# Kernel tuning notes

Hardware: AMD Instinct MI355X
Metric: run time of the kernel (lower is better)

## Reference

```python
import jax, jax.numpy as jnp
import numpy as np

H = 60.0  # self.h
C = jnp.array([10665991.0, 27000000.0, 7953253.0], dtype=jnp.float32)  # self.c (9e6*3 = 27e6)


def setup_inputs() -> dict:
    key = jax.random.key(0)
    k1, k2, k3 = jax.random.split(key, 3)
    B, T = 8192, 1024
    # room temperatures in Kelvin, strictly positive (model uses 1/x)
    x0 = 280.0 + 20.0 * jax.random.uniform(k1, (B, 3), dtype=jnp.float32)
    u = jax.random.uniform(k2, (B, T, 8), dtype=jnp.float32)
    # col 0: external temperature ~[250,300] K; cols 1..7: positive power/irradiation
    u = u.at[:, :, 0].set(250.0 + 50.0 * u[:, :, 0])
    u = u.at[:, :, 1:].multiply(1000.0)
    # 14 scalar log-conductance params: [l12, l23, le1..3, ls1..3, lh1..3, lc1..3]
    lam = 0.1 * jax.random.normal(k3, (14,), dtype=jnp.float32)
    return {"x0": x0, "u": u, "lam": lam}


def _forward(x0, u, lam):
    e = jnp.exp(lam)
    e12, e23 = e[0], e[1]
    ee, es, eh, ec = e[2:5], e[5:8], e[8:11], e[11:14]  # each [3]

    def step(x, ut):  # x: [B,3], ut: [B,8]
        inv = 1.0 / x
        d12 = inv[:, 0] - inv[:, 1]
        d23 = inv[:, 1] - inv[:, 2]
        # A @ x^T, with A's only nonzeros at (0,1),(1,0),(1,2),(2,1)
        Ax = jnp.stack([
            e12 * d12 * x[:, 1],
            -e12 * d12 * x[:, 0] + e23 * d23 * x[:, 2],
            -e23 * d23 * x[:, 1],
        ], axis=-1)  # [B,3]
        u0 = ut[:, 0:1]  # external temperature
        # B @ u_t: external exchange + solar + per-room heating (u2..4) + cooling (u5..7)
        Bu = (ee * (inv - 1.0 / u0) * u0
              + es * ut[:, 1:2]
              + eh * ut[:, 2:5]
              + ec * ut[:, 5:8])  # [B,3]
        x_new = x * jnp.exp(H * (Ax + Bu) / C)
        return x_new, x_new

    # loop runs for T-1 steps using u[:, t] for t = 0..T-2
    u_seq = jnp.swapaxes(u[:, :-1, :], 0, 1)  # [T-1, B, 8]
    _, xs = jax.lax.scan(step, x0, u_seq)
    preds_rest = jnp.swapaxes(xs, 0, 1)  # [B, T-1, 3]
    # rows where the NEXT step's external temp is ~0 are flagged with -1
    invalid = u[:, 1:, 0] < 1e-6  # [B, T-1]
    preds_rest = jnp.where(invalid[..., None], jnp.float32(-1.0), preds_rest)
    return jnp.concatenate([x0[:, None, :], preds_rest], axis=1)  # [B, T, 3]


def reference(x0, u, lam):
    return _forward(x0, u, lam)
```

## Files before the change

### kernel.cpp

```cpp
#include <hip/hip_runtime.h>


#if __has_builtin(__builtin_amdgcn_exp2f)
#define EXP2F(x) __builtin_amdgcn_exp2f(x)
#else
#define EXP2F(x) __expf((x) * 0.69314718056f)
#endif

namespace {
constexpr int T = 1024;
constexpr int SB = 16;
constexpr int NSB = T / SB;
constexpr float LOG2E = 1.4426950408889634f;
constexpr int CH_STRIDE = 132;
}

__device__ __forceinline__ float rfl(float x) {
    return __int_as_float(__builtin_amdgcn_readfirstlane(__float_as_int(x)));
}

__global__ __launch_bounds__(256, 2) void bm_fwd(
    const float* __restrict__ x0p,
    const float* __restrict__ up,
    const float* __restrict__ lamp,
    float* __restrict__ outp)
{
    __shared__ float lds[16 * CH_STRIDE];

    const int tid   = blockIdx.x * 256 + threadIdx.x;
    const int chain = tid >> 4;
    const int l     = tid & 15;
    float* __restrict__ region = lds + (threadIdx.x >> 4) * CH_STRIDE;

    float e[14];
#pragma unroll
    for (int i = 0; i < 14; ++i) e[i] = expf(lamp[i]);

    const float hc0 = (60.0f / 10665991.0f) * LOG2E;
    const float hc1 = (60.0f / 27000000.0f) * LOG2E;
    const float hc2 = (60.0f / 7953253.0f) * LOG2E;
    const float F12_0 = rfl(hc0 * e[0]), F12_1 = rfl(hc1 * e[0]);
    const float F23_1 = rfl(hc1 * e[1]), F23_2 = rfl(hc2 * e[1]);
    const float hce0 = rfl(hc0 * e[2]),  hce1 = rfl(hc1 * e[3]),  hce2 = rfl(hc2 * e[4]);
    const float ss0  = rfl(hc0 * e[5]),  ss1  = rfl(hc1 * e[6]),  ss2  = rfl(hc2 * e[7]);
    const float sh0  = rfl(hc0 * e[8]),  sh1  = rfl(hc1 * e[9]),  sh2  = rfl(hc2 * e[10]);
    const float sc0  = rfl(hc0 * e[11]), sc1  = rfl(hc1 * e[12]), sc2  = rfl(hc2 * e[13]);
    const float g0c = rfl(-hce0 - F12_0);
    const float g1c = rfl(-hce1 - F12_1 - F23_1);
    const float g2c = rfl(-hce2 - F23_2);

    float X0 = x0p[3 * chain + 0];
    float X1 = x0p[3 * chain + 1];
    float X2 = x0p[3 * chain + 2];

    const float4* __restrict__ ub = (const float4*)(up + (size_t)chain * (T * 8));
    float* __restrict__ ob = outp + (size_t)chain * (T * 3);

    auto fold_write = [&](int par, const float4& r0, const float4& r1) -> float {
        const float G0 = fmaf(sc0, r1.y, fmaf(sh0, r0.z, fmaf(ss0, r0.y, g0c)));
        const float G1 = fmaf(sc1, r1.z, fmaf(sh1, r0.w, fmaf(ss1, r0.y, g1c)));
        const float G2 = fmaf(sc2, r1.w, fmaf(sh2, r1.x, fmaf(ss2, r0.y, g2c)));
        *(float4*)(region + par * 64 + (l << 2)) = make_float4(r0.x, G0, G1, G2);
        return r0.x;
    };

    float4 pf0, pf1;
    float u0_cur;

    {
        const float4* s = ub + (size_t)(l * 2);
        float4 t0 = s[0], t1 = s[1];
        u0_cur = fold_write(0, t0, t1);
        const float4* p = ub + (size_t)((SB + l) * 2);
        pf0 = p[0]; pf1 = p[1];
    }

    for (int sb = 0; sb < NSB; ++sb) {
        const int par = sb & 1;

        const float u0_next = fold_write(par ^ 1, pf0, pf1);

        {
            const int jj = (sb + 2 < NSB) ? (sb + 2) : (NSB - 1);
            const float4* p = ub + (size_t)((jj * SB + l) * 2);
            pf0 = p[0]; pf1 = p[1];
        }

        float O0 = 0.0f, O1 = 0.0f, O2 = 0.0f;
        const float* rdbase = region + par * 64;
#pragma unroll
        for (int i = 0; i < SB; ++i) {
            const float4 r = *(const float4*)(rdbase + (i << 2));
            if (l == i) { O0 = X0; O1 = X1; O2 = X2; }
            const float i0 = __builtin_amdgcn_rcpf(X0);
            const float i1 = __builtin_amdgcn_rcpf(X1);
            const float i2 = __builtin_amdgcn_rcpf(X2);
            const float E0 = hce0 * r.x;
            const float E1 = hce1 * r.x;
            const float E2 = hce2 * r.x;
            const float p0 = fmaf(F12_0, X1, E0);
            const float p1 = fmaf(F12_1, X0, fmaf(F23_1, X2, E1));
            const float p2 = fmaf(F23_2, X1, E2);
            const float z0 = fmaf(i0, p0, r.y);
            const float z1 = fmaf(i1, p1, r.z);
            const float z2 = fmaf(i2, p2, r.w);
            X0 *= EXP2F(z0);
            X1 *= EXP2F(z1);
            X2 *= EXP2F(z2);
        }

        const int t = sb * SB + l;
        const bool bad = (u0_cur < 1e-6f) && (t != 0);
        float3 o;
        o.x = bad ? -1.0f : O0;
        o.y = bad ? -1.0f : O1;
        o.z = bad ? -1.0f : O2;
        *(float3*)(ob + (size_t)t * 3) = o;

        u0_cur = u0_next;
    }
}

extern "C" void kernel_launch(void* const* d_in, const int* in_sizes, int n_in,
                              void* d_out, int out_size, void* d_ws, size_t ws_size,
                              hipStream_t stream) {
    const float* x0  = (const float*)d_in[0];
    const float* u   = (const float*)d_in[1];
    const float* lam = (const float*)d_in[2];
    float* out = (float*)d_out;

    const int B = in_sizes[0] / 3;
    const int threads = B * 16;
    dim3 grid(threads / 256), block(256);
    hipLaunchKernelGGL(bm_fwd, grid, block, 0, stream, x0, u, lam, out);
}
```

Measured before the change: 436.0 us.

## Software-pipeline LDS reads of folded inputs into register halves across blocks

The folded per-step inputs are now read from LDS in two halves of eight float4s into registers ahead of use. Scheduling barriers pin each read early so LDS latency overlaps the serial recurrence. The next block's first half is prefetched between the two compute halves. The fold stage also precomputes hce0*u0, and the other two rooms' exchange terms are derived by scaling with constant ratios, which trims a multiply from the critical chain but adds register pressure and slight rounding changes.

After: 437.9 us. About the same (+0.4%).

```diff
diff --git a/kernel.cpp b/kernel.cpp
--- a/kernel.cpp
+++ b/kernel.cpp
@@ -48,6 +48,8 @@
     const float g0c = rfl(-hce0 - F12_0);
     const float g1c = rfl(-hce1 - F12_1 - F23_1);
     const float g2c = rfl(-hce2 - F23_2);
+    const float r10 = rfl(hce1 / hce0);
+    const float r20 = rfl(hce2 / hce0);
 
     float X0 = x0p[3 * chain + 0];
     float X1 = x0p[3 * chain + 1];
@@ -57,13 +59,43 @@
     float* __restrict__ ob = outp + (size_t)chain * (T * 3);
 
     auto fold_write = [&](int par, const float4& r0, const float4& r1) -> float {
+        const float E0 = hce0 * r0.x;
         const float G0 = fmaf(sc0, r1.y, fmaf(sh0, r0.z, fmaf(ss0, r0.y, g0c)));
         const float G1 = fmaf(sc1, r1.z, fmaf(sh1, r0.w, fmaf(ss1, r0.y, g1c)));
         const float G2 = fmaf(sc2, r1.w, fmaf(sh2, r1.x, fmaf(ss2, r0.y, g2c)));
-        *(float4*)(region + par * 64 + (l << 2)) = make_float4(r0.x, G0, G1, G2);
+        *(float4*)(region + par * 64 + (l << 2)) = make_float4(E0, G0, G1, G2);
         return r0.x;
     };
 
+    auto read_half = [&](float4 (&H)[8], int par, int half) {
+        const float* base = region + par * 64 + half * 32;
+#pragma unroll
+        for (int i = 0; i < 8; ++i) H[i] = *(const float4*)(base + (i << 2));
+    };
+
+    float O0 = 0.0f, O1 = 0.0f, O2 = 0.0f;
+
+    auto compute_half = [&](const float4 (&H)[8], int base_i) {
+#pragma unroll
+        for (int ii = 0; ii < 8; ++ii) {
+            const float4 r = H[ii];
+            if (l == base_i + ii) { O0 = X0; O1 = X1; O2 = X2; }
+            const float i0 = __builtin_amdgcn_rcpf(X0);
+            const float i1 = __builtin_amdgcn_rcpf(X1);
+            const float i2 = __builtin_amdgcn_rcpf(X2);
+            const float p0 = fmaf(F12_0, X1, r.x);
+            const float p1 = fmaf(F12_1, X0, fmaf(F23_1, X2, r10 * r.x));
+            const float p2 = fmaf(F23_2, X1, r20 * r.x);
+            const float z0 = fmaf(i0, p0, r.y);
+            const float z1 = fmaf(i1, p1, r.z);
+            const float z2 = fmaf(i2, p2, r.w);
+            X0 *= EXP2F(z0);
+            X1 *= EXP2F(z1);
+            X2 *= EXP2F(z2);
+        }
+    };
+
+    float4 H0[8], H1[8];
     float4 pf0, pf1;
     float u0_cur;
 
@@ -71,12 +103,17 @@
         const float4* s = ub + (size_t)(l * 2);
         float4 t0 = s[0], t1 = s[1];
         u0_cur = fold_write(0, t0, t1);
+        read_half(H0, 0, 0);
+        __builtin_amdgcn_sched_barrier(0);
         const float4* p = ub + (size_t)((SB + l) * 2);
         pf0 = p[0]; pf1 = p[1];
     }
 
     for (int sb = 0; sb < NSB; ++sb) {
         const int par = sb & 1;
+
+        read_half(H1, par, 1);
+        __builtin_amdgcn_sched_barrier(0);
 
         const float u0_next = fold_write(par ^ 1, pf0, pf1);
 
@@ -85,29 +122,14 @@
             const float4* p = ub + (size_t)((jj * SB + l) * 2);
             pf0 = p[0]; pf1 = p[1];
         }
+        __builtin_amdgcn_sched_barrier(0);
 
-        float O0 = 0.0f, O1 = 0.0f, O2 = 0.0f;
-        const float* rdbase = region + par * 64;
-#pragma unroll
-        for (int i = 0; i < SB; ++i) {
-            const float4 r = *(const float4*)(rdbase + (i << 2));
-            if (l == i) { O0 = X0; O1 = X1; O2 = X2; }
-            const float i0 = __builtin_amdgcn_rcpf(X0);
-            const float i1 = __builtin_amdgcn_rcpf(X1);
-            const float i2 = __builtin_amdgcn_rcpf(X2);
-            const float E0 = hce0 * r.x;
-            const float E1 = hce1 * r.x;
-            const float E2 = hce2 * r.x;
-            const float p0 = fmaf(F12_0, X1, E0);
-            const float p1 = fmaf(F12_1, X0, fmaf(F23_1, X2, E1));
-            const float p2 = fmaf(F23_2, X1, E2);
-            const float z0 = fmaf(i0, p0, r.y);
-            const float z1 = fmaf(i1, p1, r.z);
-            const float z2 = fmaf(i2, p2, r.w);
-            X0 *= EXP2F(z0);
-            X1 *= EXP2F(z1);
-            X2 *= EXP2F(z2);
-        }
+        compute_half(H0, 0);
+
+        read_half(H0, par ^ 1, 0);
+        __builtin_amdgcn_sched_barrier(0);
+
+        compute_half(H1, 8);
 
         const int t = sb * SB + l;
         const bool bad = (u0_cur < 1e-6f) && (t != 0);
```

## Replace exp2 and reciprocal with polynomial updating state and inverse

Applied to the files above, without the earlier changes.

Each step's exp2 is swapped for a degree-5 polynomial split into even and odd parts, so that 2^z and 2^-z come from the same terms. The reciprocal of the state is then tracked by multiplying by 2^-z, replacing the per-step rcp with an exact rcp once per 16-step block. The external-exchange scaling by hce0 is folded into the staging write, and the other rooms use precomputed ratios. This removes transcendental ops from the serial dependency chain, at the cost of more FMAs and possible accuracy drift if z is not small.

Measured after the change: 429.8 us. No clear change (-1.4%).

```diff
diff --git a/kernel.cpp b/kernel.cpp
--- a/kernel.cpp
+++ b/kernel.cpp
@@ -1,11 +1,5 @@
 #include <hip/hip_runtime.h>
 
-
-#if __has_builtin(__builtin_amdgcn_exp2f)
-#define EXP2F(x) __builtin_amdgcn_exp2f(x)
-#else
-#define EXP2F(x) __expf((x) * 0.69314718056f)
-#endif
 
 namespace {
 constexpr int T = 1024;
@@ -13,6 +7,11 @@
 constexpr int NSB = T / SB;
 constexpr float LOG2E = 1.4426950408889634f;
 constexpr int CH_STRIDE = 132;
+constexpr float PC1 = 0.69314718055994531f;
+constexpr float PC2 = 0.24022650695910072f;
+constexpr float PC3 = 0.05550410866482158f;
+constexpr float PC4 = 0.00961812910762848f;
+constexpr float PC5 = 0.00133335581464284f;
 }
 
 __device__ __forceinline__ float rfl(float x) {
@@ -48,20 +47,34 @@
     const float g0c = rfl(-hce0 - F12_0);
     const float g1c = rfl(-hce1 - F12_1 - F23_1);
     const float g2c = rfl(-hce2 - F23_2);
+    const float r10 = rfl(hce1 / hce0);
+    const float r20 = rfl(hce2 / hce0);
 
     float X0 = x0p[3 * chain + 0];
     float X1 = x0p[3 * chain + 1];
     float X2 = x0p[3 * chain + 2];
+    float I0 = __builtin_amdgcn_rcpf(X0);
+    float I1 = __builtin_amdgcn_rcpf(X1);
+    float I2 = __builtin_amdgcn_rcpf(X2);
 
     const float4* __restrict__ ub = (const float4*)(up + (size_t)chain * (T * 8));
     float* __restrict__ ob = outp + (size_t)chain * (T * 3);
 
     auto fold_write = [&](int par, const float4& r0, const float4& r1) -> float {
+        const float E0 = hce0 * r0.x;
         const float G0 = fmaf(sc0, r1.y, fmaf(sh0, r0.z, fmaf(ss0, r0.y, g0c)));
         const float G1 = fmaf(sc1, r1.z, fmaf(sh1, r0.w, fmaf(ss1, r0.y, g1c)));
         const float G2 = fmaf(sc2, r1.w, fmaf(sh2, r1.x, fmaf(ss2, r0.y, g2c)));
-        *(float4*)(region + par * 64 + (l << 2)) = make_float4(r0.x, G0, G1, G2);
+        *(float4*)(region + par * 64 + (l << 2)) = make_float4(E0, G0, G1, G2);
         return r0.x;
+    };
+
+    auto pstep = [](float z, float& X, float& I) {
+        const float z2 = z * z;
+        const float ev = fmaf(fmaf(PC4, z2, PC2), z2, 1.0f);
+        const float od = z * fmaf(fmaf(PC5, z2, PC3), z2, PC1);
+        X *= (ev + od);
+        I *= (ev - od);
     };
 
     float4 pf0, pf1;
@@ -92,22 +105,21 @@
         for (int i = 0; i < SB; ++i) {
             const float4 r = *(const float4*)(rdbase + (i << 2));
             if (l == i) { O0 = X0; O1 = X1; O2 = X2; }
-            const float i0 = __builtin_amdgcn_rcpf(X0);
-            const float i1 = __builtin_amdgcn_rcpf(X1);
-            const float i2 = __builtin_amdgcn_rcpf(X2);
-            const float E0 = hce0 * r.x;
-            const float E1 = hce1 * r.x;
-            const float E2 = hce2 * r.x;
+            const float E0 = r.x;
             const float p0 = fmaf(F12_0, X1, E0);
-            const float p1 = fmaf(F12_1, X0, fmaf(F23_1, X2, E1));
-            const float p2 = fmaf(F23_2, X1, E2);
-            const float z0 = fmaf(i0, p0, r.y);
-            const float z1 = fmaf(i1, p1, r.z);
-            const float z2 = fmaf(i2, p2, r.w);
-            X0 *= EXP2F(z0);
-            X1 *= EXP2F(z1);
-            X2 *= EXP2F(z2);
+            const float p1 = fmaf(F12_1, X0, fmaf(F23_1, X2, r10 * E0));
+            const float p2 = fmaf(F23_2, X1, r20 * E0);
+            const float z0 = fmaf(I0, p0, r.y);
+            const float z1 = fmaf(I1, p1, r.z);
+            const float z2 = fmaf(I2, p2, r.w);
+            pstep(z0, X0, I0);
+            pstep(z1, X1, I1);
+            pstep(z2, X2, I2);
         }
+
+        I0 = __builtin_amdgcn_rcpf(X0);
+        I1 = __builtin_amdgcn_rcpf(X1);
+        I2 = __builtin_amdgcn_rcpf(X2);
 
         const int t = sb * SB + l;
         const bool bad = (u0_cur < 1e-6f) && (t != 0);
```
